# Kernel tuning notes

Measured on AMD Instinct MI355X. Metric: run time of the kernel, lower is better.

The kernel has to match this reference:

```python
import jax, jax.numpy as jnp
import numpy as np

FEAT_DIM = 512
NUM_CLASS = 100000
N = 512
M = 0.5
S = 64.0
COS_M = float(np.cos(M))
SIN_M = float(np.sin(M))
THRESHOLD = float(np.cos(np.pi - M))
MM = float(np.sin(np.pi - M) * M)
LABEL_SMOOTH = 0.1


def setup_inputs() -> dict:
    key = jax.random.key(0)
    k1, k2, k3 = jax.random.split(key, 3)
    embbedings = jax.random.normal(k1, (N, FEAT_DIM), dtype=jnp.float32)
    label = jax.random.randint(k2, (N,), 0, NUM_CLASS, dtype=jnp.int64 if jax.config.jax_enable_x64 else jnp.int32)
    w = 0.01 * jax.random.normal(k3, (FEAT_DIM, NUM_CLASS), dtype=jnp.float32)
    return {"embbedings": embbedings, "w": w, "label": label}


def reference(embbedings, w, label):
    n = embbedings.shape[0]
    rows = jnp.arange(n)

    # weight column-normalize (done with no_grad in torch) and feature row-normalize
    wn = w / jnp.linalg.norm(w, axis=0, keepdims=True)
    e = embbedings / jnp.linalg.norm(embbedings, axis=1, keepdims=True)

    cos_theta = jnp.clip(e @ wn, -1.0, 1.0)          # [N, C]
    target_logit = cos_theta[rows, label][:, None]    # [N, 1]

    sin_theta = jnp.sqrt(1.0 - target_logit ** 2)
    cos_theta_m = target_logit * COS_M - sin_theta * SIN_M  # cos(theta + m)

    mask = cos_theta > cos_theta_m                    # hard examples
    final_target_logit = jnp.where(target_logit > THRESHOLD,
                                   cos_theta_m, target_logit - MM)

    # adaptive t (running buffer starts at 0 -> single-step value), no grad in torch
    t = jax.lax.stop_gradient(0.01 * jnp.mean(target_logit))

    cos_theta = jnp.where(mask, cos_theta * (t + cos_theta), cos_theta)
    cos_theta = cos_theta.at[rows, label].set(final_target_logit[:, 0])

    logits = cos_theta * S
    logp = jax.nn.log_softmax(logits, axis=-1)
    nll = -logp[rows, label]
    smooth = -jnp.mean(logp, axis=-1)  # eps/C * sum_c(-logp) == eps * mean(-logp)
    loss = jnp.mean((1.0 - LABEL_SMOOTH) * nll + LABEL_SMOOTH * smooth)
    return loss
```

## Files before the change

kernel.cpp:

```cpp
#include <hip/hip_runtime.h>

#define KD    512
#define NCLS  100000
#define BC    64
#define NB    ((NCLS + BC - 1) / BC)
#define R1B   64
#define R1C   25
#define S_SCALE 64.0f
#define COS_M   0.87758256189037276f
#define SIN_M   0.47942553860420301f
#define THRESH (-0.87758256189037276f)
#define MM_C    0.23971276930210151f

typedef __attribute__((ext_vector_type(8))) short short8;
typedef __attribute__((ext_vector_type(4))) float f32x4;

union Pack8 { unsigned short u[8]; uint4 v; };

__device__ __forceinline__ unsigned short f2bf(float x) {
  unsigned int u = __float_as_uint(x);
  u += 0x7fffu + ((u >> 16) & 1u);
  return (unsigned short)(u >> 16);
}

__global__ void k0_norm_target(const float* __restrict__ emb, const float* __restrict__ w,
                               const int* __restrict__ label,
                               unsigned short* __restrict__ eb, float* __restrict__ tlA) {
  int r = blockIdx.x;
  int l = threadIdx.x;
  const float* src = emb + (size_t)r * KD + l * 8;
  float v[8];
  float ss = 0.f;
#pragma unroll
  for (int j = 0; j < 8; ++j) { v[j] = src[j]; ss += v[j] * v[j]; }
#pragma unroll
  for (int m = 1; m < 64; m <<= 1) ss += __shfl_xor(ss, m, 64);
  float rn = rsqrtf(ss);
  Pack8 p;
#pragma unroll
  for (int j = 0; j < 8; ++j) {
    float x = v[j] * rn;
    v[j] = x;
    p.u[j] = f2bf(x);
  }
  *reinterpret_cast<uint4*>(eb + (size_t)r * KD + l * 8) = p.v;

  int lab = label[r];
  float wv[8];
#pragma unroll
  for (int j = 0; j < 8; ++j) wv[j] = w[(size_t)(l * 8 + j) * NCLS + lab];
  float dot = 0.f, sq = 0.f;
#pragma unroll
  for (int j = 0; j < 8; ++j) { dot += v[j] * wv[j]; sq += wv[j] * wv[j]; }
#pragma unroll
  for (int m = 1; m < 64; m <<= 1) {
    dot += __shfl_xor(dot, m, 64);
    sq  += __shfl_xor(sq, m, 64);
  }
  if (l == 0) {
    float tl = dot * rsqrtf(sq);
    tlA[r] = fminf(1.f, fmaxf(-1.f, tl));
  }
}

__global__ void k_prep(const float* __restrict__ tlA, float* __restrict__ ctmA,
                       float* __restrict__ finA, float* __restrict__ tval) {
  __shared__ float red[512];
  int i = threadIdx.x;
  float tl = tlA[i];
  red[i] = tl;
  __syncthreads();
  for (int s = 256; s > 0; s >>= 1) {
    if (i < s) red[i] += red[i + s];
    __syncthreads();
  }
  float st = sqrtf(fmaxf(0.f, 1.f - tl * tl));
  float ctm = tl * COS_M - st * SIN_M;
  ctmA[i] = ctm;
  finA[i] = (tl > THRESH) ? ctm : (tl - MM_C);
  if (i == 0) tval[0] = 0.01f * red[0] * (1.f / 512.f);
}

__global__ __launch_bounds__(256, 2)
void k_gemm(const float* __restrict__ w, const unsigned short* __restrict__ eb,
            const int* __restrict__ label, const float* __restrict__ ctmA,
            const float* __restrict__ finA, const float* __restrict__ tval,
            float2* __restrict__ part) {
  __shared__ __align__(16) unsigned short Bs[BC * KD];
  __shared__ float ssW[4][BC];
  __shared__ float invnS[BC];
  __shared__ float sE[512];
  __shared__ float sL[512];
  const int tid = threadIdx.x;
  const int wv = tid >> 6;
  const int l  = tid & 63;
  const int c0 = blockIdx.x * BC;

  {
    const int c = l;
    const int cgc = (c0 + c < NCLS) ? (c0 + c) : (NCLS - 1);
    const float* wp = w + cgc;
    float ss = 0.f;
#pragma unroll 1
    for (int ph = 0; ph < 2; ++ph) {
      float vb[8][8];
#pragma unroll
      for (int b = 0; b < 8; ++b) {
        const int kb = wv * 8 + (ph * 8 + b) * 32;
#pragma unroll
        for (int j = 0; j < 8; ++j)
          vb[b][j] = __builtin_nontemporal_load(&wp[(size_t)(kb + j) * NCLS]);
      }
      __builtin_amdgcn_sched_barrier(0);
#pragma unroll
      for (int b = 0; b < 8; ++b) {
        const int kb = wv * 8 + (ph * 8 + b) * 32;
        Pack8 p;
#pragma unroll
        for (int j = 0; j < 8; ++j) {
          float x = vb[b][j];
          ss += x * x;
          p.u[j] = f2bf(x);
        }
        const int G = c * 64 + ((kb >> 3) ^ (c & 7));
        *reinterpret_cast<uint4*>(&Bs[G * 8]) = p.v;
      }
    }
    ssW[wv][c] = ss;
  }
  __syncthreads();
  if (tid < BC) {
    float s = ssW[0][tid] + ssW[1][tid] + ssW[2][tid] + ssW[3][tid];
    invnS[tid] = (s > 0.f) ? rsqrtf(s) : 0.f;
  }
  __syncthreads();

  const int q  = l >> 4;
  const int cl = l & 15;
  const int rbase = wv * 128;
  f32x4 acc[8][4] = {};

#pragma unroll 1
  for (int s = 0; s < 16; ++s) {
    const int k0 = s * 32 + q * 8;
    short8 a[8], b[4];
#pragma unroll
    for (int ct = 0; ct < 4; ++ct) {
      int c = ct * 16 + cl;
      int G = c * 64 + ((k0 >> 3) ^ (c & 7));
      b[ct] = *reinterpret_cast<const short8*>(&Bs[G * 8]);
    }
#pragma unroll
    for (int rt = 0; rt < 8; ++rt) {
      int row = rbase + rt * 16 + cl;
      a[rt] = *reinterpret_cast<const short8*>(eb + (size_t)row * KD + k0);
    }
#pragma unroll
    for (int rt = 0; rt < 8; ++rt)
#pragma unroll
      for (int ct = 0; ct < 4; ++ct)
        acc[rt][ct] = __builtin_amdgcn_mfma_f32_16x16x32_bf16(a[rt], b[ct], acc[rt][ct], 0, 0, 0);
  }

  const float t = tval[0];
#pragma unroll
  for (int rt = 0; rt < 8; ++rt) {
#pragma unroll
    for (int rg = 0; rg < 4; ++rg) {
      const int row = rbase + rt * 16 + q * 4 + rg;
      const float ctm = ctmA[row];
      const float fin = finA[row];
      const int   lab = label[row];
      float se = 0.f, sl = 0.f;
#pragma unroll
      for (int ct = 0; ct < 4; ++ct) {
        const int cg = c0 + ct * 16 + cl;
        if (cg < NCLS) {
          float cosv = acc[rt][ct][rg] * invnS[ct * 16 + cl];
          cosv = fminf(1.f, fmaxf(-1.f, cosv));
          float logit = (cosv > ctm) ? cosv * (t + cosv) : cosv;
          if (cg == lab) logit = fin;
          float x = S_SCALE * logit;
          se += __expf(x);
          sl += x;
        }
      }
#pragma unroll
      for (int m = 1; m < 16; m <<= 1) {
        se += __shfl_xor(se, m, 64);
        sl += __shfl_xor(sl, m, 64);
      }
      if (cl == 0) { sE[row] = se; sL[row] = sl; }
    }
  }
  __syncthreads();

  {
    float2* dst = part + (size_t)blockIdx.x * 512;
    dst[tid]       = make_float2(sE[tid],       sL[tid]);
    dst[tid + 256] = make_float2(sE[tid + 256], sL[tid + 256]);
  }
}

__global__ void k_reduce1(const float2* __restrict__ part, float2* __restrict__ part2) {
  const int j = blockIdx.x;
  const int r = threadIdx.x;
  const int i0 = j * R1C;
  const int i1 = (i0 + R1C < NB) ? (i0 + R1C) : NB;
  float se = 0.f, sl = 0.f;
  for (int i = i0; i < i1; ++i) {
    float2 p = part[(size_t)i * 512 + r];
    se += p.x; sl += p.y;
  }
  part2[(size_t)j * 512 + r] = make_float2(se, sl);
}

__global__ void k_loss(const float2* __restrict__ part2, const float* __restrict__ finA,
                       float* __restrict__ out) {
  __shared__ float red[512];
  const int r = threadIdx.x;
  float se = 0.f, sl = 0.f;
#pragma unroll 4
  for (int j = 0; j < R1B; ++j) {
    float2 p = part2[(size_t)j * 512 + r];
    se += p.x; sl += p.y;
  }
  float lse = logf(se);
  float nll = lse - S_SCALE * finA[r];
  float sm  = lse - sl * (1.f / (float)NCLS);
  red[r] = 0.9f * nll + 0.1f * sm;
  __syncthreads();
  for (int s = 256; s > 0; s >>= 1) {
    if (r < s) red[r] += red[r + s];
    __syncthreads();
  }
  if (r == 0) out[0] = red[0] * (1.f / 512.f);
}

extern "C" void kernel_launch(void* const* d_in, const int* in_sizes, int n_in,
                              void* d_out, int out_size, void* d_ws, size_t ws_size,
                              hipStream_t stream) {
  (void)in_sizes; (void)n_in; (void)out_size; (void)ws_size;
  const float* emb = (const float*)d_in[0];
  const float* w   = (const float*)d_in[1];
  const int*   lab = (const int*)d_in[2];
  float* out = (float*)d_out;

  char* ws = (char*)d_ws;
  unsigned short* eb = (unsigned short*)ws;
  float* tlA   = (float*)(ws + 524288);
  float* ctmA  = tlA  + 512;
  float* finA  = ctmA + 512;
  float* tval  = finA + 512;
  float2* part  = (float2*)(ws + 524288 + 8192);
  float2* part2 = part + (size_t)NB * 512;

  hipLaunchKernelGGL(k0_norm_target, dim3(512), dim3(64), 0, stream, emb, w, lab, eb, tlA);
  hipLaunchKernelGGL(k_prep,    dim3(1),   dim3(512), 0, stream, tlA, ctmA, finA, tval);
  hipLaunchKernelGGL(k_gemm,    dim3(NB),  dim3(256), 0, stream,
                     w, eb, lab, ctmA, finA, tval, part);
  hipLaunchKernelGGL(k_reduce1, dim3(R1B), dim3(512), 0, stream, part, part2);
  hipLaunchKernelGGL(k_loss,    dim3(1),   dim3(512), 0, stream, part2, finA, out);
}
```

Measured before the change: 448.4 us.

## Pre-convert weights to MFMA-tiled bf16 layout in a separate kernel

Adds a kernel that reads the fp32 weight matrix once, converts it to bf16 in a tiled layout that matches the MFMA B-operand fragment order, and writes partial column sums of squares. The GEMM kernel then loads B fragments straight from global memory instead of staging strided fp32 columns through LDS. This takes the strided weight loads and the LDS traffic out of the GEMM and lets the grid spread the conversion across more blocks. The cost is an extra write and re-read of about 100MB of bf16 weights, plus a large workspace requirement; if the workspace is too small, the old kernel is used instead.

After: 489.9 us. 9.3% more time.

```diff
diff --git a/kernel.cpp b/kernel.cpp
--- a/kernel.cpp
+++ b/kernel.cpp
@@ -4,6 +4,8 @@
 #define NCLS  100000
 #define BC    64
 #define NB    ((NCLS + BC - 1) / BC)
+#define NTILE 1564
+#define CPAD  100096
 #define R1B   64
 #define R1C   25
 #define S_SCALE 64.0f
@@ -81,8 +83,129 @@
   if (i == 0) tval[0] = 0.01f * red[0] * (1.f / 512.f);
 }
 
+__global__ __launch_bounds__(256)
+void k_w(const float* __restrict__ w, unsigned short* __restrict__ wb,
+         float* __restrict__ sqpart) {
+  const int tid = threadIdx.x;
+  const int ch  = blockIdx.x >> 2;
+  const int kh  = blockIdx.x & 3;
+  const int c   = ch * 256 + tid;
+  const int cc  = (c < NCLS) ? c : (NCLS - 1);
+  const bool valid = (c < NCLS);
+  const int cb = c >> 6;
+  const int ct = (c >> 4) & 3;
+  const int cl = c & 15;
+  unsigned short* gdst = wb + (size_t)cb * 32768 + ct * 128 + cl * 8;
+  const float* srcc = w + cc;
+  float sq = 0.f;
+#pragma unroll 2
+  for (int o16 = 0; o16 < 16; ++o16) {
+    const int o = kh * 16 + o16;
+    float v[8];
+#pragma unroll
+    for (int j = 0; j < 8; ++j)
+      v[j] = srcc[(size_t)(o * 8 + j) * NCLS];
+    Pack8 p;
+#pragma unroll
+    for (int j = 0; j < 8; ++j) {
+      float x = valid ? v[j] : 0.f;
+      sq += x * x;
+      p.u[j] = f2bf(x);
+    }
+    *reinterpret_cast<uint4*>(gdst + (size_t)o * 512) = p.v;
+  }
+  sqpart[(size_t)kh * CPAD + c] = sq;
+}
+
 __global__ __launch_bounds__(256, 2)
-void k_gemm(const float* __restrict__ w, const unsigned short* __restrict__ eb,
+void k_gemm(const unsigned short* __restrict__ wb, const float* __restrict__ sqpart,
+            const unsigned short* __restrict__ eb,
+            const int* __restrict__ label, const float* __restrict__ ctmA,
+            const float* __restrict__ finA, const float* __restrict__ tval,
+            float2* __restrict__ part) {
+  __shared__ float invnS[BC];
+  __shared__ float sE[512];
+  __shared__ float sL[512];
+  const int tid = threadIdx.x;
+  const int wv = tid >> 6;
+  const int l  = tid & 63;
+  const int c0 = blockIdx.x * BC;
+
+  if (tid < BC) {
+    const int c = c0 + tid;
+    float s = sqpart[0 * (size_t)CPAD + c] + sqpart[1 * (size_t)CPAD + c]
+            + sqpart[2 * (size_t)CPAD + c] + sqpart[3 * (size_t)CPAD + c];
+    invnS[tid] = (s > 0.f) ? rsqrtf(s) : 0.f;
+  }
+  __syncthreads();
+
+  const int q  = l >> 4;
+  const int cl = l & 15;
+  const int rbase = wv * 128;
+  const unsigned short* bt = wb + (size_t)blockIdx.x * 32768 + q * 512 + cl * 8;
+  f32x4 acc[8][4] = {};
+
+#pragma unroll 1
+  for (int s = 0; s < 16; ++s) {
+    const int k0 = s * 32 + q * 8;
+    short8 a[8], b[4];
+#pragma unroll
+    for (int ct = 0; ct < 4; ++ct)
+      b[ct] = *reinterpret_cast<const short8*>(bt + s * 2048 + ct * 128);
+#pragma unroll
+    for (int rt = 0; rt < 8; ++rt) {
+      int row = rbase + rt * 16 + cl;
+      a[rt] = *reinterpret_cast<const short8*>(eb + (size_t)row * KD + k0);
+    }
+#pragma unroll
+    for (int rt = 0; rt < 8; ++rt)
+#pragma unroll
+      for (int ct = 0; ct < 4; ++ct)
+        acc[rt][ct] = __builtin_amdgcn_mfma_f32_16x16x32_bf16(a[rt], b[ct], acc[rt][ct], 0, 0, 0);
+  }
+
+  const float t = tval[0];
+#pragma unroll
+  for (int rt = 0; rt < 8; ++rt) {
+#pragma unroll
+    for (int rg = 0; rg < 4; ++rg) {
+      const int row = rbase + rt * 16 + q * 4 + rg;
+      const float ctm = ctmA[row];
+      const float fin = finA[row];
+      const int   lab = label[row];
+      float se = 0.f, sl = 0.f;
+#pragma unroll
+      for (int ct = 0; ct < 4; ++ct) {
+        const int cg = c0 + ct * 16 + cl;
+        if (cg < NCLS) {
+          float cosv = acc[rt][ct][rg] * invnS[ct * 16 + cl];
+          cosv = fminf(1.f, fmaxf(-1.f, cosv));
+          float logit = (cosv > ctm) ? cosv * (t + cosv) : cosv;
+          if (cg == lab) logit = fin;
+          float x = S_SCALE * logit;
+          se += __expf(x);
+          sl += x;
+        }
+      }
+#pragma unroll
+      for (int m = 1; m < 16; m <<= 1) {
+        se += __shfl_xor(se, m, 64);
+        sl += __shfl_xor(sl, m, 64);
+      }
+      if (cl == 0) { sE[row] = se; sL[row] = sl; }
+    }
+  }
+  __syncthreads();
+
+  {
+    float2* dst = part + (size_t)blockIdx.x * 512;
+    dst[tid]       = make_float2(sE[tid],       sL[tid]);
+    dst[tid + 256] = make_float2(sE[tid + 256], sL[tid + 256]);
+  }
+}
+
+__global__ __launch_bounds__(256, 2)
+void k_gemm_legacy(const float* __restrict__ w, const unsigned short* __restrict__ eb,
             const int* __restrict__ label, const float* __restrict__ ctmA,
             const float* __restrict__ finA, const float* __restrict__ tval,
             float2* __restrict__ part) {
@@ -95,7 +218,6 @@
   const int wv = tid >> 6;
   const int l  = tid & 63;
   const int c0 = blockIdx.x * BC;
-
   {
     const int c = l;
     const int cgc = (c0 + c < NCLS) ? (c0 + c) : (NCLS - 1);
@@ -134,12 +256,10 @@
     invnS[tid] = (s > 0.f) ? rsqrtf(s) : 0.f;
   }
   __syncthreads();
-
   const int q  = l >> 4;
   const int cl = l & 15;
   const int rbase = wv * 128;
   f32x4 acc[8][4] = {};
-
 #pragma unroll 1
   for (int s = 0; s < 16; ++s) {
     const int k0 = s * 32 + q * 8;
@@ -161,7 +281,6 @@
       for (int ct = 0; ct < 4; ++ct)
         acc[rt][ct] = __builtin_amdgcn_mfma_f32_16x16x32_bf16(a[rt], b[ct], acc[rt][ct], 0, 0, 0);
   }
-
   const float t = tval[0];
 #pragma unroll
   for (int rt = 0; rt < 8; ++rt) {
@@ -194,7 +313,6 @@
     }
   }
   __syncthreads();
-
   {
     float2* dst = part + (size_t)blockIdx.x * 512;
     dst[tid]       = make_float2(sE[tid],       sL[tid]);
@@ -240,7 +358,7 @@
 extern "C" void kernel_launch(void* const* d_in, const int* in_sizes, int n_in,
                               void* d_out, int out_size, void* d_ws, size_t ws_size,
                               hipStream_t stream) {
-  (void)in_sizes; (void)n_in; (void)out_size; (void)ws_size;
+  (void)in_sizes; (void)n_in; (void)out_size;
   const float* emb = (const float*)d_in[0];
   const float* w   = (const float*)d_in[1];
   const int*   lab = (const int*)d_in[2];
@@ -254,11 +372,23 @@
   float* tval  = finA + 512;
   float2* part  = (float2*)(ws + 524288 + 8192);
   float2* part2 = part + (size_t)NB * 512;
-
-  hipLaunchKernelGGL(k0_norm_target, dim3(512), dim3(64), 0, stream, emb, w, lab, eb, tlA);
-  hipLaunchKernelGGL(k_prep,    dim3(1),   dim3(512), 0, stream, tlA, ctmA, finA, tval);
-  hipLaunchKernelGGL(k_gemm,    dim3(NB),  dim3(256), 0, stream,
-                     w, eb, lab, ctmA, finA, tval, part);
+  const size_t wb_off = 7196672;
+  unsigned short* wb = (unsigned short*)(ws + wb_off);
+  float* sqpart = (float*)(ws + wb_off + (size_t)NTILE * 65536);
+  const size_t need = wb_off + (size_t)NTILE * 65536 + (size_t)4 * CPAD * 4;
+
+  if (ws_size >= need) {
+    hipLaunchKernelGGL(k_w,  dim3(1564), dim3(256), 0, stream, w, wb, sqpart);
+    hipLaunchKernelGGL(k0_norm_target, dim3(512), dim3(64), 0, stream, emb, w, lab, eb, tlA);
+    hipLaunchKernelGGL(k_prep, dim3(1), dim3(512), 0, stream, tlA, ctmA, finA, tval);
+    hipLaunchKernelGGL(k_gemm, dim3(NB), dim3(256), 0, stream,
+                       wb, sqpart, eb, lab, ctmA, finA, tval, part);
+  } else {
+    hipLaunchKernelGGL(k0_norm_target, dim3(512), dim3(64), 0, stream, emb, w, lab, eb, tlA);
+    hipLaunchKernelGGL(k_prep, dim3(1), dim3(512), 0, stream, tlA, ctmA, finA, tval);
+    hipLaunchKernelGGL(k_gemm_legacy, dim3(NB), dim3(256), 0, stream,
+                       w, eb, lab, ctmA, finA, tval, part);
+  }
   hipLaunchKernelGGL(k_reduce1, dim3(R1B), dim3(512), 0, stream, part, part2);
   hipLaunchKernelGGL(k_loss,    dim3(1),   dim3(512), 0, stream, part2, finA, out);
 }
```
